# Optimization experiments

Hardware: AMD Instinct MI355X
Metric: run time of the kernel (lower is better)

The kernel has to match this reference:

```python
import jax, jax.numpy as jnp
import numpy as np
import math

B, L, S, H, E, D = 4, 2048, 2048, 8, 64, 64


def setup_inputs() -> dict:
    key = jax.random.key(0)
    kq, kk, kv = jax.random.split(key, 3)
    queries = jax.random.normal(kq, (B, L, H, E), dtype=jnp.float32)
    keys = jax.random.normal(kk, (B, S, H, E), dtype=jnp.float32)
    values = jax.random.normal(kv, (B, S, H, D), dtype=jnp.float32)
    # TriangularCausalMask: True above the diagonal = masked out
    attn_mask = jnp.triu(jnp.ones((L, S), dtype=bool), k=1)[None, None]  # [1,1,L,S]
    return {"queries": queries, "keys": keys, "values": values, "attn_mask": attn_mask}


def reference(queries, keys, values, attn_mask):
    # queries [B,L,H,E], keys [B,S,H,E], values [B,S,H,D], attn_mask bool [1,1,L,S]
    scale = 1.0 / math.sqrt(queries.shape[-1])
    scores = jnp.einsum('blhe,bshe->bhls', queries, keys)  # [B,H,L,S]
    scores = jnp.where(attn_mask, -jnp.inf, scores)
    A = jax.nn.softmax(scale * scores, axis=-1)  # dropout p=0.0 -> identity
    V = jnp.einsum('bhls,bshd->blhd', A, values)  # [B,L,H,D]
    return V
```

## Files before the change

kernel.cpp:

```cpp
#include <hip/hip_runtime.h>


typedef unsigned short u16;
typedef unsigned int   u32;
typedef short short8   __attribute__((ext_vector_type(8)));
typedef float floatx16 __attribute__((ext_vector_type(16)));
typedef u32 u32x4      __attribute__((ext_vector_type(4)));

#define B_ 4
#define L_ 2048
#define S_ 2048
#define H_ 8
#define E_ 64
#define D_ 64

static __device__ __forceinline__ u32 pack2(float lo, float hi) {
    const u32 a = __float_as_uint(lo) + 0x8000u;
    const u32 b = __float_as_uint(hi) + 0x8000u;
    return __builtin_amdgcn_perm(b, a, 0x07060302u);
}
static __device__ __forceinline__ u16 bf16c(float x) {
    return (u16)((__float_as_uint(x) + 0x8000u) >> 16);
}
static __device__ __forceinline__ void pl32swap(u32& a, u32& b) {
    asm("v_permlane32_swap_b32 %0, %1" : "+v"(a), "+v"(b));
}
static __device__ __forceinline__ floatx16 zero16() {
    floatx16 z;
    #pragma unroll
    for (int i = 0; i < 16; i++) z[i] = 0.f;
    return z;
}
static __device__ __forceinline__ void gload_lds16(u16* lds, const u16* g) {
    __builtin_amdgcn_global_load_lds((const __attribute__((address_space(1))) void*)g,
                                     (__attribute__((address_space(3))) void*)lds,
                                     16, 0, 0);
}

__global__ __launch_bounds__(256)
void cvt_kernel(const float* __restrict__ k, const float* __restrict__ v,
                u16* __restrict__ kc, u16* __restrict__ vt)
{
    __shared__ u16 Lt[64 * 72];
    const int bx = blockIdx.x, t = threadIdx.x;
    const int tile = bx & 1023;
    const int kt = tile & 31, h = (tile >> 5) & 7, b = tile >> 8;
    const int F  = t >> 5;
    const int hi = (t >> 4) & 1;
    const int l0 = (t & 15) * 2;

    if (bx < 1024) {
        const int mt = F >> 2, ks = F & 3;
        const int s  = kt * 64 + mt * 32 + l0;
        const int e  = ks * 16 + hi * 8;
        const float* p0 = k + (((size_t)(b * S_ + s)) * H_ + h) * E_ + e;
        const float4 a0 = ((const float4*)p0)[0], a1 = ((const float4*)p0)[1];
        const float* p1 = p0 + H_ * E_;
        const float4 b0 = ((const float4*)p1)[0], b1 = ((const float4*)p1)[1];
        u16* dst = kc + ((size_t)(b * 8 + h)) * 131072 + (size_t)kt * 4096 + t * 16;
        *(u32x4*)dst = (u32x4){pack2(a0.x, a0.y), pack2(a0.z, a0.w),
                               pack2(a1.x, a1.y), pack2(a1.z, a1.w)};
        *(u32x4*)(dst + 8) = (u32x4){pack2(b0.x, b0.y), pack2(b0.z, b0.w),
                                     pack2(b1.x, b1.y), pack2(b1.z, b1.w)};
    } else {
        {
            const int i  = t >> 2;
            const int d0 = (t & 3) * 16;
            const float* vp = v + (((size_t)(b * S_ + kt * 64 + i)) * H_ + h) * D_ + d0;
            const float4 a0 = ((const float4*)vp)[0], a1 = ((const float4*)vp)[1];
            const float4 a2 = ((const float4*)vp)[2], a3 = ((const float4*)vp)[3];
            const float va[16] = {a0.x,a0.y,a0.z,a0.w, a1.x,a1.y,a1.z,a1.w,
                                  a2.x,a2.y,a2.z,a2.w, a3.x,a3.y,a3.z,a3.w};
            #pragma unroll
            for (int jj = 0; jj < 16; jj++) Lt[(d0 + jj) * 72 + i] = bf16c(va[jj]);
        }
        __syncthreads();
        {
            const int nt = F >> 2, ks = F & 3;
            const int d1 = nt * 32 + l0;
            u16* dst = vt + ((size_t)(b * 8 + h)) * 131072 + (size_t)kt * 4096 + t * 16;
            *(u32x4*)dst       = *(const u32x4*)&Lt[(d1    ) * 72 + ks * 16 + hi * 8];
            *(u32x4*)(dst + 8) = *(const u32x4*)&Lt[(d1 + 1) * 72 + ks * 16 + hi * 8];
        }
    }
}

template<int SRC>
__global__ __launch_bounds__(128, 2)
void fa_kernel(const float* __restrict__ q, const float* __restrict__ kk,
               const float* __restrict__ vv, const u16* __restrict__ kc,
               const u16* __restrict__ vt, float* __restrict__ out)
{
    __shared__ __align__(16) u16 KV[2][8192];

    const int tid  = threadIdx.x;
    const int w    = tid >> 6;
    const int lane = tid & 63;
    const int l31  = lane & 31;
    const int hi   = lane >> 5;

    const int bx   = blockIdx.x;
    const int h    = bx & 7;
    const int b    = (bx >> 3) & 3;
    const int idx  = bx >> 5;
    const int t    = (idx < 16) ? (31 - idx) : (idx - 16);
    const int q0   = 64 * t + 32 * w;
    const int ktend = t;

    const float kscale = 0.18033688011112042f;

    const float* qptr = q + (((size_t)b * L_ + q0 + l31) * H_ + h) * E_ + hi * 8;
    short8 qf[4];
    #pragma unroll
    for (int ks = 0; ks < 4; ks++) {
        const float4 a0 = *(const float4*)(qptr + ks * 16);
        const float4 a1 = *(const float4*)(qptr + ks * 16 + 4);
        const u32x4 u = {pack2(a0.x * kscale, a0.y * kscale), pack2(a0.z * kscale, a0.w * kscale),
                         pack2(a1.x * kscale, a1.y * kscale), pack2(a1.z * kscale, a1.w * kscale)};
        qf[ks] = __builtin_bit_cast(short8, u);
    }

    const size_t bh = (size_t)(b * 8 + h);
    const u16* kcb = kc + bh * 131072;
    const u16* vtb = vt + bh * 131072;

    auto stage = [&](int kt, int bufi) {
        #pragma unroll
        for (int ff = 0; ff < 4; ff++) {
            const int f = w * 4 + ff;
            gload_lds16(&KV[bufi][f * 512],        kcb + (size_t)kt * 4096 + f * 512 + lane * 8);
            gload_lds16(&KV[bufi][4096 + f * 512], vtb + (size_t)kt * 4096 + f * 512 + lane * 8);
        }
    };
    auto stage_sync = [&](int kt) {
        #pragma unroll
        for (int ff = 0; ff < 4; ff++) {
            const int f = w * 4 + ff;
            const int mt = f >> 2, ks = f & 3;
            const float* p = kk + (((size_t)b * S_ + kt * 64 + mt * 32 + l31) * H_ + h) * E_ + ks * 16 + hi * 8;
            const float4 a0 = *(const float4*)p;
            const float4 a1 = *(const float4*)(p + 4);
            *(u32x4*)&KV[0][f * 512 + lane * 8] =
                (u32x4){pack2(a0.x, a0.y), pack2(a0.z, a0.w), pack2(a1.x, a1.y), pack2(a1.z, a1.w)};
            float fv[8];
            #pragma unroll
            for (int jj = 0; jj < 8; jj++)
                fv[jj] = vv[(((size_t)b * S_ + kt * 64 + ks * 16 + hi * 8 + jj) * H_ + h) * D_ + mt * 32 + l31];
            *(u32x4*)&KV[0][4096 + f * 512 + lane * 8] =
                (u32x4){pack2(fv[0], fv[1]), pack2(fv[2], fv[3]), pack2(fv[4], fv[5]), pack2(fv[6], fv[7])};
        }
    };

    floatx16 occ[2] = {zero16(), zero16()};
    float m_run = -1e30f, l_run = 0.f;

    if constexpr (SRC == 0) {
        stage(0, 0);
        asm volatile("s_waitcnt vmcnt(0)" ::: "memory");
        __builtin_amdgcn_s_barrier();
        __builtin_amdgcn_sched_barrier(0);
    }

    for (int kt = 0; kt <= ktend; kt++) {
        int cur;
        if constexpr (SRC == 0) {
            cur = kt & 1;
            if (kt < ktend) {
                stage(kt + 1, cur ^ 1);
                asm volatile("s_waitcnt vmcnt(8)" ::: "memory");
            } else {
                asm volatile("s_waitcnt vmcnt(0)" ::: "memory");
            }
            __builtin_amdgcn_s_barrier();
            __builtin_amdgcn_sched_barrier(0);
        } else {
            cur = 0;
            stage_sync(kt);
            __syncthreads();
        }

        short8 kfr[2][4], vfr[2][4];
        #pragma unroll
        for (int mt = 0; mt < 2; mt++)
            #pragma unroll
            for (int ks = 0; ks < 4; ks++) {
                kfr[mt][ks] = *(const short8*)&KV[cur][(mt * 4 + ks) * 512 + lane * 8];
                vfr[mt][ks] = *(const short8*)&KV[cur][4096 + (mt * 4 + ks) * 512 + lane * 8];
            }

        floatx16 sac[2];
        __builtin_amdgcn_s_setprio(1);
        #pragma unroll
        for (int mt = 0; mt < 2; mt++) {
            floatx16 c = zero16();
            #pragma unroll
            for (int ks = 0; ks < 4; ks++)
                c = __builtin_amdgcn_mfma_f32_32x32x16_bf16(kfr[mt][ks], qf[ks], c, 0, 0, 0);
            sac[mt] = c;
        }
        __builtin_amdgcn_s_setprio(0);

        if (kt == ktend) {
            const int qg = q0 + l31;
            #pragma unroll
            for (int mt = 0; mt < 2; mt++)
                #pragma unroll
                for (int r = 0; r < 16; r++) {
                    const int keyg = kt * 64 + mt * 32 + (r & 3) + (r >> 2) * 8 + hi * 4;
                    if (keyg > qg) sac[mt][r] = -1e30f;
                }
        }

        float red[16];
        #pragma unroll
        for (int r = 0; r < 16; r++) red[r] = fmaxf(sac[0][r], sac[1][r]);
        #pragma unroll
        for (int stp = 8; stp > 0; stp >>= 1)
            #pragma unroll
            for (int r = 0; r < stp; r++) red[r] = fmaxf(red[r], red[r + stp]);
        const float mx = fmaxf(red[0], __shfl_xor(red[0], 32));

        const bool defer = __all(mx - m_run <= 8.0f) != 0;
        if (!defer) {
            const float mnew  = fmaxf(m_run, mx);
            const float alpha = exp2f(m_run - mnew);
            m_run = mnew;
            l_run *= alpha;
            #pragma unroll
            for (int r = 0; r < 16; r++) { occ[0][r] *= alpha; occ[1][r] *= alpha; }
        }

        float sum[16];
        #pragma unroll
        for (int r = 0; r < 16; r++) {
            sac[0][r] = exp2f(sac[0][r] - m_run);
            sac[1][r] = exp2f(sac[1][r] - m_run);
            sum[r] = sac[0][r] + sac[1][r];
        }
        #pragma unroll
        for (int stp = 8; stp > 0; stp >>= 1)
            #pragma unroll
            for (int r = 0; r < stp; r++) sum[r] += sum[r + stp];
        l_run += sum[0] + __shfl_xor(sum[0], 32);

        u32 pk0[8], pk1[8];
        #pragma unroll
        for (int r2 = 0; r2 < 4; r2++) {
            pk0[2 * r2 + 0] = pack2(sac[0][4 * r2 + 0], sac[0][4 * r2 + 1]);
            pk0[2 * r2 + 1] = pack2(sac[0][4 * r2 + 2], sac[0][4 * r2 + 3]);
            pk1[2 * r2 + 0] = pack2(sac[1][4 * r2 + 0], sac[1][4 * r2 + 1]);
            pk1[2 * r2 + 1] = pack2(sac[1][4 * r2 + 2], sac[1][4 * r2 + 3]);
        }

        __builtin_amdgcn_s_setprio(1);
        #pragma unroll
        for (int ks = 0; ks < 4; ks++) {
            const int u = (ks & 1) * 4;
            u32 w0, w1, w2, w3;
            if (ks < 2) { w0 = pk0[u]; w1 = pk0[u + 1]; w2 = pk0[u + 2]; w3 = pk0[u + 3]; }
            else        { w0 = pk1[u]; w1 = pk1[u + 1]; w2 = pk1[u + 2]; w3 = pk1[u + 3]; }
            pl32swap(w0, w2);
            pl32swap(w1, w3);
            const u32x4 pw = {w0, w1, w2, w3};
            const short8 pf = __builtin_bit_cast(short8, pw);
            occ[0] = __builtin_amdgcn_mfma_f32_32x32x16_bf16(vfr[0][ks], pf, occ[0], 0, 0, 0);
            occ[1] = __builtin_amdgcn_mfma_f32_32x32x16_bf16(vfr[1][ks], pf, occ[1], 0, 0, 0);
        }
        __builtin_amdgcn_s_setprio(0);

        if constexpr (SRC == 0) {
            __builtin_amdgcn_sched_barrier(0);
            __builtin_amdgcn_s_barrier();
        } else {
            __syncthreads();
        }
    }

    const float inv = 1.0f / l_run;
    float* op = out + (((size_t)b * L_ + q0 + l31) * H_ + h) * D_;
    #pragma unroll
    for (int nt = 0; nt < 2; nt++)
        #pragma unroll
        for (int r2 = 0; r2 < 4; r2++) {
            const float4 o = {occ[nt][4 * r2 + 0] * inv, occ[nt][4 * r2 + 1] * inv,
                              occ[nt][4 * r2 + 2] * inv, occ[nt][4 * r2 + 3] * inv};
            *(float4*)(op + nt * 32 + r2 * 8 + hi * 4) = o;
        }
}

extern "C" void kernel_launch(void* const* d_in, const int* in_sizes, int n_in,
                              void* d_out, int out_size, void* d_ws, size_t ws_size,
                              hipStream_t stream) {
    const float* q = (const float*)d_in[0];
    const float* k = (const float*)d_in[1];
    const float* v = (const float*)d_in[2];
    float* out = (float*)d_out;

    const size_t elems = (size_t)B_ * H_ * S_ * E_;
    const size_t need  = elems * 2 * 2;
    if (d_ws != nullptr && ws_size >= need) {
        u16* kc = (u16*)d_ws;
        u16* vt = kc + elems;
        cvt_kernel<<<dim3(2048), dim3(256), 0, stream>>>(k, v, kc, vt);
        fa_kernel<0><<<dim3(1024), dim3(128), 0, stream>>>(q, k, v, kc, vt, out);
    } else {
        fa_kernel<1><<<dim3(1024), dim3(128), 0, stream>>>(q, k, v, nullptr, nullptr, out);
    }
}
```

Measured before the change: 159.2 us.

## Split KV range across waves per query block and merge partial softmax in LDS

Each block now handles 32 query rows with 4 waves. Each wave processes a contiguous chunk of the causal KV tiles, so 2048 blocks of 256 threads replace 1024 blocks of 128. K and V fragments are loaded straight from global memory into registers, dropping the LDS double-buffer staging and the per-tile barriers. Partial accumulators, running max and running sum are then combined through LDS in a two-step tree merge. This aims to raise parallelism and balance the causal workload, at the cost of doubled global/L2 traffic for K/V, no explicit prefetch, and extra merge work.

```diff
diff --git a/kernel.cpp b/kernel.cpp
--- a/kernel.cpp
+++ b/kernel.cpp
@@ -30,11 +30,6 @@
     #pragma unroll
     for (int i = 0; i < 16; i++) z[i] = 0.f;
     return z;
-}
-static __device__ __forceinline__ void gload_lds16(u16* lds, const u16* g) {
-    __builtin_amdgcn_global_load_lds((const __attribute__((address_space(1))) void*)g,
-                                     (__attribute__((address_space(3))) void*)lds,
-                                     16, 0, 0);
 }
 
 __global__ __launch_bounds__(256)
@@ -86,12 +81,12 @@
 }
 
 template<int SRC>
-__global__ __launch_bounds__(128, 2)
+__global__ __launch_bounds__(256, 4)
 void fa_kernel(const float* __restrict__ q, const float* __restrict__ kk,
                const float* __restrict__ vv, const u16* __restrict__ kc,
                const u16* __restrict__ vt, float* __restrict__ out)
 {
-    __shared__ __align__(16) u16 KV[2][8192];
+    __shared__ float Ms[2][2176];
 
     const int tid  = threadIdx.x;
     const int w    = tid >> 6;
@@ -102,10 +97,14 @@
     const int bx   = blockIdx.x;
     const int h    = bx & 7;
     const int b    = (bx >> 3) & 3;
-    const int idx  = bx >> 5;
-    const int t    = (idx < 16) ? (31 - idx) : (idx - 16);
-    const int q0   = 64 * t + 32 * w;
-    const int ktend = t;
+    const int ss   = bx >> 5;
+    const int s    = 63 - ss;
+    const int T    = (s >> 1) + 1;
+    const int Tm1  = T - 1;
+    const int q0   = 32 * s;
+    const int C    = (T + 3) >> 2;
+    const int kt0  = w * C;
+    const int kt1  = min(kt0 + C, T);
 
     const float kscale = 0.18033688011112042f;
 
@@ -124,69 +123,41 @@
     const u16* kcb = kc + bh * 131072;
     const u16* vtb = vt + bh * 131072;
 
-    auto stage = [&](int kt, int bufi) {
-        #pragma unroll
-        for (int ff = 0; ff < 4; ff++) {
-            const int f = w * 4 + ff;
-            gload_lds16(&KV[bufi][f * 512],        kcb + (size_t)kt * 4096 + f * 512 + lane * 8);
-            gload_lds16(&KV[bufi][4096 + f * 512], vtb + (size_t)kt * 4096 + f * 512 + lane * 8);
-        }
-    };
-    auto stage_sync = [&](int kt) {
-        #pragma unroll
-        for (int ff = 0; ff < 4; ff++) {
-            const int f = w * 4 + ff;
-            const int mt = f >> 2, ks = f & 3;
+    auto loadK = [&](int kt, int mt, int ks) -> short8 {
+        if constexpr (SRC == 0) {
+            const u32x4 u = *(const u32x4*)&kcb[(size_t)kt * 4096 + (mt * 4 + ks) * 512 + lane * 8];
+            return __builtin_bit_cast(short8, u);
+        } else {
             const float* p = kk + (((size_t)b * S_ + kt * 64 + mt * 32 + l31) * H_ + h) * E_ + ks * 16 + hi * 8;
             const float4 a0 = *(const float4*)p;
             const float4 a1 = *(const float4*)(p + 4);
-            *(u32x4*)&KV[0][f * 512 + lane * 8] =
-                (u32x4){pack2(a0.x, a0.y), pack2(a0.z, a0.w), pack2(a1.x, a1.y), pack2(a1.z, a1.w)};
-            float fv[8];
+            const u32x4 u = {pack2(a0.x, a0.y), pack2(a0.z, a0.w), pack2(a1.x, a1.y), pack2(a1.z, a1.w)};
+            return __builtin_bit_cast(short8, u);
+        }
+    };
+    auto loadV = [&](int kt, int nt, int ks) -> short8 {
+        if constexpr (SRC == 0) {
+            const u32x4 u = *(const u32x4*)&vtb[(size_t)kt * 4096 + (nt * 4 + ks) * 512 + lane * 8];
+            return __builtin_bit_cast(short8, u);
+        } else {
+            float f[8];
             #pragma unroll
             for (int jj = 0; jj < 8; jj++)
-                fv[jj] = vv[(((size_t)b * S_ + kt * 64 + ks * 16 + hi * 8 + jj) * H_ + h) * D_ + mt * 32 + l31];
-            *(u32x4*)&KV[0][4096 + f * 512 + lane * 8] =
-                (u32x4){pack2(fv[0], fv[1]), pack2(fv[2], fv[3]), pack2(fv[4], fv[5]), pack2(fv[6], fv[7])};
+                f[jj] = vv[(((size_t)b * S_ + kt * 64 + ks * 16 + hi * 8 + jj) * H_ + h) * D_ + nt * 32 + l31];
+            const u32x4 u = {pack2(f[0], f[1]), pack2(f[2], f[3]), pack2(f[4], f[5]), pack2(f[6], f[7])};
+            return __builtin_bit_cast(short8, u);
         }
     };
 
     floatx16 occ[2] = {zero16(), zero16()};
     float m_run = -1e30f, l_run = 0.f;
 
-    if constexpr (SRC == 0) {
-        stage(0, 0);
-        asm volatile("s_waitcnt vmcnt(0)" ::: "memory");
-        __builtin_amdgcn_s_barrier();
-        __builtin_amdgcn_sched_barrier(0);
-    }
-
-    for (int kt = 0; kt <= ktend; kt++) {
-        int cur;
-        if constexpr (SRC == 0) {
-            cur = kt & 1;
-            if (kt < ktend) {
-                stage(kt + 1, cur ^ 1);
-                asm volatile("s_waitcnt vmcnt(8)" ::: "memory");
-            } else {
-                asm volatile("s_waitcnt vmcnt(0)" ::: "memory");
-            }
-            __builtin_amdgcn_s_barrier();
-            __builtin_amdgcn_sched_barrier(0);
-        } else {
-            cur = 0;
-            stage_sync(kt);
-            __syncthreads();
-        }
-
-        short8 kfr[2][4], vfr[2][4];
+    for (int kt = kt0; kt < kt1; kt++) {
+        short8 kfr[2][4];
         #pragma unroll
         for (int mt = 0; mt < 2; mt++)
             #pragma unroll
-            for (int ks = 0; ks < 4; ks++) {
-                kfr[mt][ks] = *(const short8*)&KV[cur][(mt * 4 + ks) * 512 + lane * 8];
-                vfr[mt][ks] = *(const short8*)&KV[cur][4096 + (mt * 4 + ks) * 512 + lane * 8];
-            }
+            for (int ks = 0; ks < 4; ks++) kfr[mt][ks] = loadK(kt, mt, ks);
 
         floatx16 sac[2];
         __builtin_amdgcn_s_setprio(1);
@@ -200,7 +171,13 @@
         }
         __builtin_amdgcn_s_setprio(0);
 
-        if (kt == ktend) {
+        short8 vfr[2][4];
+        #pragma unroll
+        for (int nt = 0; nt < 2; nt++)
+            #pragma unroll
+            for (int ks = 0; ks < 4; ks++) vfr[nt][ks] = loadV(kt, nt, ks);
+
+        if (kt == Tm1) {
             const int qg = q0 + l31;
             #pragma unroll
             for (int mt = 0; mt < 2; mt++)
@@ -267,25 +244,49 @@
             occ[1] = __builtin_amdgcn_mfma_f32_32x32x16_bf16(vfr[1][ks], pf, occ[1], 0, 0, 0);
         }
         __builtin_amdgcn_s_setprio(0);
-
-        if constexpr (SRC == 0) {
-            __builtin_amdgcn_sched_barrier(0);
-            __builtin_amdgcn_s_barrier();
-        } else {
-            __syncthreads();
-        }
-    }
-
-    const float inv = 1.0f / l_run;
-    float* op = out + (((size_t)b * L_ + q0 + l31) * H_ + h) * D_;
-    #pragma unroll
-    for (int nt = 0; nt < 2; nt++)
-        #pragma unroll
-        for (int r2 = 0; r2 < 4; r2++) {
-            const float4 o = {occ[nt][4 * r2 + 0] * inv, occ[nt][4 * r2 + 1] * inv,
-                              occ[nt][4 * r2 + 2] * inv, occ[nt][4 * r2 + 3] * inv};
-            *(float4*)(op + nt * 32 + r2 * 8 + hi * 4) = o;
-        }
+    }
+
+    auto dump = [&](int slot) {
+        #pragma unroll
+        for (int nt = 0; nt < 2; nt++)
+            #pragma unroll
+            for (int r = 0; r < 16; r++) Ms[slot][(nt * 16 + r) * 64 + lane] = occ[nt][r];
+        Ms[slot][2048 + lane] = m_run;
+        Ms[slot][2112 + lane] = l_run;
+    };
+    auto mergeIn = [&](int slot) {
+        const float mB = Ms[slot][2048 + lane], lB = Ms[slot][2112 + lane];
+        const float m  = fmaxf(m_run, mB);
+        const float aA = exp2f(m_run - m), aB = exp2f(mB - m);
+        m_run = m;
+        l_run = l_run * aA + lB * aB;
+        #pragma unroll
+        for (int nt = 0; nt < 2; nt++)
+            #pragma unroll
+            for (int r = 0; r < 16; r++)
+                occ[nt][r] = occ[nt][r] * aA + Ms[slot][(nt * 16 + r) * 64 + lane] * aB;
+    };
+
+    __syncthreads();
+    if (w == 1 || w == 3) dump(w >> 1);
+    __syncthreads();
+    if (w == 0 || w == 2) mergeIn(w >> 1);
+    __syncthreads();
+    if (w == 2) dump(1);
+    __syncthreads();
+    if (w == 0) {
+        mergeIn(1);
+        const float inv = 1.0f / l_run;
+        float* op = out + (((size_t)b * L_ + q0 + l31) * H_ + h) * D_;
+        #pragma unroll
+        for (int nt = 0; nt < 2; nt++)
+            #pragma unroll
+            for (int r2 = 0; r2 < 4; r2++) {
+                const float4 o = {occ[nt][4 * r2 + 0] * inv, occ[nt][4 * r2 + 1] * inv,
+                                  occ[nt][4 * r2 + 2] * inv, occ[nt][4 * r2 + 3] * inv};
+                *(float4*)(op + nt * 32 + r2 * 8 + hi * 4) = o;
+            }
+    }
 }
 
 extern "C" void kernel_launch(void* const* d_in, const int* in_sizes, int n_in,
@@ -302,8 +303,8 @@
         u16* kc = (u16*)d_ws;
         u16* vt = kc + elems;
         cvt_kernel<<<dim3(2048), dim3(256), 0, stream>>>(k, v, kc, vt);
-        fa_kernel<0><<<dim3(1024), dim3(128), 0, stream>>>(q, k, v, kc, vt, out);
+        fa_kernel<0><<<dim3(2048), dim3(256), 0, stream>>>(q, k, v, kc, vt, out);
     } else {
-        fa_kernel<1><<<dim3(1024), dim3(128), 0, stream>>>(q, k, v, nullptr, nullptr, out);
-    }
-}
+        fa_kernel<1><<<dim3(2048), dim3(256), 0, stream>>>(q, k, v, nullptr, nullptr, out);
+    }
+}
```

Measured after the change: 156.9 us. No clear change (-1.4%).
